# Kernel tuning notes

Measured on AMD Instinct MI355X. Metric: run time of the kernel, lower is better.

## Reference

```python
import jax, jax.numpy as jnp
import numpy as np

NUM_NODES = 100000
PROP_STEP = 8


def _spmm(vals, rows, cols, x):
    # sparse [N,N] @ dense [N,F]: gather source rows, scale, scatter-add to dest
    gathered = x[cols] * vals[:, None]  # [E, F]
    return jax.ops.segment_sum(gathered, rows, num_segments=NUM_NODES)


def setup_inputs() -> dict:
    key = jax.random.key(0)
    k1, k2, k3, k4, k5 = jax.random.split(key, 5)
    N, E, C = NUM_NODES, 3200000, 128
    x = jax.random.normal(k1, (N, C), dtype=jnp.float32)
    # xavier_uniform for weight [c_in, c_out]
    limit = float(np.sqrt(6.0 / (C + C)))
    weight = jax.random.uniform(k2, (C, C), dtype=jnp.float32, minval=-limit, maxval=limit)
    lap_vals = jax.random.uniform(k3, (E,), dtype=jnp.float32)
    lap_rows = jax.random.randint(k4, (E,), 0, N, dtype=jnp.int64)
    lap_cols = jax.random.randint(k5, (E,), 0, N, dtype=jnp.int64)
    return {"x": x, "weight": weight, "lap_vals": lap_vals,
            "lap_rows": lap_rows, "lap_cols": lap_cols}


def reference(x, weight, lap_vals, lap_rows, lap_cols):
    # filter_type='low', dropout inactive (eval / p=0)
    identity = x
    out = x @ weight  # [N, c_out]
    for _ in range(PROP_STEP):
        out = _spmm(lap_vals, lap_rows, lap_cols, out)
    return identity + out
```

## Files before the change

### kernel.cpp

```cpp
#include <hip/hip_runtime.h>
#include <hip/hip_bf16.h>
#include <hip/hip_fp16.h>
#include <stdint.h>

#define CCH 128
#define FINAL_SCALE 268435456.0f
#define RND 2048
#define BUKSH 9
#define BUKROWS 512
#define MAXBUK 256
#define COLMASK 0x1FFFF


__global__ __launch_bounds__(256) void bucket_hist_kernel(const int* __restrict__ rows,
                                                          int* __restrict__ bukcnt,
                                                          int E, int nbuk) {
    __shared__ int h[MAXBUK];
    for (int i = threadIdx.x; i < nbuk; i += 256) h[i] = 0;
    __syncthreads();
    int stride = gridDim.x * blockDim.x;
    for (int e = blockIdx.x * blockDim.x + threadIdx.x; e < E; e += stride)
        atomicAdd(&h[rows[e] >> BUKSH], 1);
    __syncthreads();
    for (int i = threadIdx.x; i < nbuk; i += 256)
        if (h[i]) atomicAdd(&bukcnt[i], h[i]);
}

__global__ __launch_bounds__(MAXBUK) void bucket_scan_kernel(const int* __restrict__ bukcnt,
                                                             int* __restrict__ bukptr,
                                                             int* __restrict__ gcur, int nbuk) {
    __shared__ int tile[MAXBUK];
    int t = threadIdx.x;
    tile[t] = (t < nbuk) ? bukcnt[t] : 0;
    __syncthreads();
    for (int off = 1; off < MAXBUK; off <<= 1) {
        int add = (t >= off) ? tile[t - off] : 0;
        __syncthreads();
        tile[t] += add;
        __syncthreads();
    }
    int excl = (t == 0) ? 0 : tile[t - 1];
    if (t < nbuk) {
        bukptr[t] = excl;
        gcur[t] = excl;
    }
    if (t == nbuk - 1) bukptr[nbuk] = tile[t];
}

__global__ __launch_bounds__(256) void part_kernel(const int* __restrict__ rows,
                                                   const int* __restrict__ cols,
                                                   const float* __restrict__ vals,
                                                   int* __restrict__ gcur,
                                                   unsigned int* __restrict__ rec_rc,
                                                   float* __restrict__ rec_v,
                                                   int E, int nbuk) {
    __shared__ int hist[MAXBUK];
    __shared__ int offs[MAXBUK];
    __shared__ int cur[MAXBUK];
    __shared__ int gbase[MAXBUK];
    __shared__ unsigned int stage_rc[RND];
    __shared__ float stage_v[RND];
    __shared__ unsigned char stage_b[RND];

    int base = blockIdx.x * RND;
    int cnt = E - base;
    if (cnt > RND) cnt = RND;
    if (cnt <= 0) return;

    for (int i = threadIdx.x; i < nbuk; i += 256) hist[i] = 0;
    __syncthreads();

    int myr[RND / 256], myc[RND / 256];
    float myv[RND / 256];
#pragma unroll
    for (int k = 0; k < RND / 256; ++k) {
        int li = k * 256 + threadIdx.x;
        bool ok = li < cnt;
        int gi = base + li;
        myr[k] = ok ? rows[gi] : -1;
        myc[k] = ok ? cols[gi] : 0;
        myv[k] = ok ? vals[gi] : 0.f;
        if (ok) atomicAdd(&hist[myr[k] >> BUKSH], 1);
    }
    __syncthreads();

    if (threadIdx.x == 0) {
        int run = 0;
        for (int b = 0; b < nbuk; ++b) {
            offs[b] = run;
            cur[b] = run;
            run += hist[b];
        }
    }
    __syncthreads();
    if (threadIdx.x < nbuk) gbase[threadIdx.x] = atomicAdd(&gcur[threadIdx.x], hist[threadIdx.x]);
    __syncthreads();

#pragma unroll
    for (int k = 0; k < RND / 256; ++k) {
        if (myr[k] >= 0) {
            int b = myr[k] >> BUKSH;
            int p = atomicAdd(&cur[b], 1);
            stage_rc[p] = ((unsigned int)(myr[k] & (BUKROWS - 1)) << 17) | (unsigned int)myc[k];
            stage_v[p] = myv[k];
            stage_b[p] = (unsigned char)b;
        }
    }
    __syncthreads();

    for (int i = threadIdx.x; i < cnt; i += 256) {
        int b = stage_b[i];
        size_t d = (size_t)gbase[b] + (i - offs[b]);
        rec_rc[d] = stage_rc[i];
        rec_v[d] = stage_v[i];
    }
}

__global__ __launch_bounds__(512) void csrfill2_kernel(const unsigned int* __restrict__ rec_rc,
                                                       const float* __restrict__ rec_v,
                                                       const int* __restrict__ bukptr,
                                                       int* __restrict__ row_ptr,
                                                       int2* __restrict__ edges,
                                                       int n, int E) {
    __shared__ int lcnt[BUKROWS];
    __shared__ int lscan[BUKROWS];
    __shared__ int lfill[BUKROWS];
    int bucket = blockIdx.x;
    int r0 = bucket << BUKSH;
    if (r0 >= n) return;
    int t = threadIdx.x;
    int bstart = bukptr[bucket];
    int bend = bukptr[bucket + 1];

    lcnt[t] = 0;
    __syncthreads();

    for (int i = bstart + t; i < bend; i += 512)
        atomicAdd(&lcnt[rec_rc[i] >> 17], 1);
    __syncthreads();

    int v = lcnt[t];
    lscan[t] = v;
    __syncthreads();
    for (int off = 1; off < 512; off <<= 1) {
        int add = (t >= off) ? lscan[t - off] : 0;
        __syncthreads();
        lscan[t] += add;
        __syncthreads();
    }
    int excl = lscan[t] - v;

    int r = r0 + t;
    if (r < n) row_ptr[r] = bstart + excl;
    if (bucket == 0 && t == 0) row_ptr[n] = E;

    lfill[t] = 0;
    lcnt[t] = bstart + excl;
    __syncthreads();

    int i = bstart + t;
    for (; i + 512 < bend; i += 1024) {
        unsigned int wa = rec_rc[i];
        unsigned int wb = rec_rc[i + 512];
        float va = rec_v[i];
        float vb = rec_v[i + 512];
        int ra = wa >> 17, rb = wb >> 17;
        int pa = lcnt[ra] + atomicAdd(&lfill[ra], 1);
        int pb = lcnt[rb] + atomicAdd(&lfill[rb], 1);
        edges[pa] = make_int2((int)(wa & COLMASK), __float_as_int(va));
        edges[pb] = make_int2((int)(wb & COLMASK), __float_as_int(vb));
    }
    if (i < bend) {
        unsigned int wa = rec_rc[i];
        float va = rec_v[i];
        int ra = wa >> 17;
        int pa = lcnt[ra] + atomicAdd(&lfill[ra], 1);
        edges[pa] = make_int2((int)(wa & COLMASK), __float_as_int(va));
    }
}


#define GEMM_ROWS 64

__global__ __launch_bounds__(256) void gemm_kernel(const float* __restrict__ x,
                                                   const float* __restrict__ w,
                                                   __half* __restrict__ out, int n) {
    __shared__ __half2 wl[CCH * 64];
    for (int i = threadIdx.x; i < CCH * 64 / 2; i += 256) {
        float4 v = ((const float4*)w)[i];
        wl[2 * i]     = __float22half2_rn(make_float2(v.x, v.y));
        wl[2 * i + 1] = __float22half2_rn(make_float2(v.z, v.w));
    }
    __syncthreads();

    int tc = threadIdx.x & 31;
    int tr = threadIdx.x >> 5;
    int rbase = blockIdx.x * GEMM_ROWS + tr * 8;
    int nr = n - rbase;
    if (nr > 8) nr = 8;
    if (nr <= 0) nr = 0;

    float acc[8][4] = {};
    const float* xp = x + (size_t)rbase * CCH;

    float4 xc[8];
#pragma unroll
    for (int j = 0; j < 8; ++j)
        xc[j] = (j < nr) ? *(const float4*)(xp + (size_t)j * CCH)
                         : make_float4(0.f, 0.f, 0.f, 0.f);

    for (int k = 0; k < CCH; k += 4) {
        float4 xn[8];
        if (k + 4 < CCH) {
#pragma unroll
            for (int j = 0; j < 8; ++j)
                xn[j] = (j < nr) ? *(const float4*)(xp + (size_t)j * CCH + k + 4)
                                 : make_float4(0.f, 0.f, 0.f, 0.f);
        }
#pragma unroll
        for (int kk = 0; kk < 4; ++kk) {
            __half2 w01 = wl[(k + kk) * 64 + tc * 2];
            __half2 w23 = wl[(k + kk) * 64 + tc * 2 + 1];
            float2 f01 = __half22float2(w01);
            float2 f23 = __half22float2(w23);
#pragma unroll
            for (int j = 0; j < 8; ++j) {
                float xs = (kk == 0) ? xc[j].x : (kk == 1) ? xc[j].y : (kk == 2) ? xc[j].z : xc[j].w;
                acc[j][0] += xs * f01.x;
                acc[j][1] += xs * f01.y;
                acc[j][2] += xs * f23.x;
                acc[j][3] += xs * f23.y;
            }
        }
        if (k + 4 < CCH) {
#pragma unroll
            for (int j = 0; j < 8; ++j) xc[j] = xn[j];
        }
    }
#pragma unroll
    for (int j = 0; j < 8; ++j)
        if (j < nr) {
            __half2* orow = (__half2*)(out + (size_t)(rbase + j) * CCH + tc * 4);
            orow[0] = __float22half2_rn(make_float2(acc[j][0], acc[j][1]));
            orow[1] = __float22half2_rn(make_float2(acc[j][2], acc[j][3]));
        }
}


template <int FINAL>
__global__ __launch_bounds__(256) void spmm_kernel(const int* __restrict__ row_ptr,
                                                   const int2* __restrict__ edges,
                                                   const __half* __restrict__ src,
                                                   __half* __restrict__ dsth,
                                                   float* __restrict__ dstf,
                                                   const float* __restrict__ identity,
                                                   int n) {
    int lane = threadIdx.x & 63;
    int row = (blockIdx.x * blockDim.x + threadIdx.x) >> 6;
    if (row >= n) return;
    int g = lane >> 4;
    int gl = lane & 15;

    int s = row_ptr[row];
    int e = row_ptr[row + 1];

    float acc[8] = {};

    for (int base = s; base < e; base += 16) {
        int2 ed[4];
        float4 gv[4];
#pragma unroll
        for (int t = 0; t < 4; ++t) {
            int idx = base + g * 4 + t;
            bool ok = idx < e;
            ed[t] = edges[ok ? idx : s];
            if (!ok) ed[t].y = 0;
        }
#pragma unroll
        for (int t = 0; t < 4; ++t)
            gv[t] = *(const float4*)(src + (size_t)ed[t].x * CCH + gl * 8);
#pragma unroll
        for (int t = 0; t < 4; ++t) {
            float v = __int_as_float(ed[t].y);
            const __half* h = (const __half*)&gv[t];
#pragma unroll
            for (int j = 0; j < 8; ++j)
                acc[j] += v * __half2float(h[j]);
        }
    }

#pragma unroll
    for (int j = 0; j < 8; ++j) {
        acc[j] += __shfl_xor(acc[j], 16, 64);
        acc[j] += __shfl_xor(acc[j], 32, 64);
    }

    if (FINAL) {
        if (g == 0) {
            const float* iv = identity + (size_t)row * CCH + gl * 8;
            float4 o;
            o.x = iv[0] + acc[0] * FINAL_SCALE;
            o.y = iv[1] + acc[1] * FINAL_SCALE;
            o.z = iv[2] + acc[2] * FINAL_SCALE;
            o.w = iv[3] + acc[3] * FINAL_SCALE;
            *(float4*)(dstf + (size_t)row * CCH + gl * 8) = o;
        } else if (g == 1) {
            const float* iv = identity + (size_t)row * CCH + gl * 8 + 4;
            float4 o;
            o.x = iv[0] + acc[4] * FINAL_SCALE;
            o.y = iv[1] + acc[5] * FINAL_SCALE;
            o.z = iv[2] + acc[6] * FINAL_SCALE;
            o.w = iv[3] + acc[7] * FINAL_SCALE;
            *(float4*)(dstf + (size_t)row * CCH + gl * 8 + 4) = o;
        }
    } else {
        if (g == 0) {
            __half2 h[4];
            h[0] = __float22half2_rn(make_float2(acc[0] * 0.0625f, acc[1] * 0.0625f));
            h[1] = __float22half2_rn(make_float2(acc[2] * 0.0625f, acc[3] * 0.0625f));
            h[2] = __float22half2_rn(make_float2(acc[4] * 0.0625f, acc[5] * 0.0625f));
            h[3] = __float22half2_rn(make_float2(acc[6] * 0.0625f, acc[7] * 0.0625f));
            *(float4*)(dsth + (size_t)row * CCH + gl * 8) = *(float4*)h;
        }
    }
}


static inline size_t align256(size_t x) { return (x + 255) & ~(size_t)255; }

extern "C" void kernel_launch(void* const* d_in, const int* in_sizes, int n_in,
                              void* d_out, int out_size, void* d_ws, size_t ws_size,
                              hipStream_t stream) {
    const float* x = (const float*)d_in[0];
    const float* w = (const float*)d_in[1];
    const float* lap_vals = (const float*)d_in[2];
    const int* lap_rows = (const int*)d_in[3];
    const int* lap_cols = (const int*)d_in[4];

    const int N = in_sizes[0] / CCH;
    const int E = in_sizes[2];
    const int NBUK = (N + BUKROWS - 1) >> BUKSH;

    char* ws = (char*)d_ws;
    size_t off = 0;
    __half* bufA = (__half*)(ws + off); off = align256(off + (size_t)N * CCH * sizeof(__half));
    __half* bufB = (__half*)(ws + off); off = align256(off + (size_t)N * CCH * sizeof(__half));
    int2* edges = (int2*)(ws + off);    off = align256(off + (size_t)E * sizeof(int2) + 16);
    int* row_ptr = (int*)(ws + off);    off = align256(off + (size_t)(N + 1) * sizeof(int));
    int* bukcnt = (int*)(ws + off);     off = align256(off + (size_t)MAXBUK * sizeof(int));
    int* bukptr = (int*)(ws + off);     off = align256(off + (size_t)(MAXBUK + 1) * sizeof(int));
    int* gcur = (int*)(ws + off);       off = align256(off + (size_t)MAXBUK * sizeof(int));
    (void)ws_size;
    unsigned int* rec_rc = (unsigned int*)bufA;
    float* rec_v = (float*)(rec_rc + E);

    float* out = (float*)d_out;

    hipMemsetAsync(bukcnt, 0, (size_t)MAXBUK * sizeof(int), stream);

    bucket_hist_kernel<<<512, 256, 0, stream>>>(lap_rows, bukcnt, E, NBUK);
    bucket_scan_kernel<<<1, MAXBUK, 0, stream>>>(bukcnt, bukptr, gcur, NBUK);
    part_kernel<<<(E + RND - 1) / RND, 256, 0, stream>>>(lap_rows, lap_cols, lap_vals,
                                                         gcur, rec_rc, rec_v, E, NBUK);
    csrfill2_kernel<<<NBUK, 512, 0, stream>>>(rec_rc, rec_v, bukptr, row_ptr, edges, N, E);

    gemm_kernel<<<(N + GEMM_ROWS - 1) / GEMM_ROWS, 256, 0, stream>>>(x, w, bufA, N);

    int spmm_blocks = (N + 3) / 4;
    const __half* src = bufA;
    __half* dst = bufB;
    for (int step = 1; step <= 7; ++step) {
        spmm_kernel<0><<<spmm_blocks, 256, 0, stream>>>(row_ptr, edges, src, dst, nullptr, nullptr, N);
        __half* t = (__half*)src;
        src = dst;
        dst = t;
    }
    spmm_kernel<1><<<spmm_blocks, 256, 0, stream>>>(row_ptr, edges, src, nullptr, out, x, N);
}
```

Measured before the change: 1.135 ms.

## Split SpMM feature dimension into two half-width passes per step

Each propagation step now launches the SpMM kernel twice, each pass gathering and writing only 64 of the 128 fp16 feature channels. This halves the size of the gathered working set per pass, aiming for better cache hit rates on the random row gathers. In exchange the CSR row pointers and edge list are read twice per step, launch count doubles, and each gather becomes an 8-byte load instead of 16 bytes.

```diff
diff --git a/kernel.cpp b/kernel.cpp
--- a/kernel.cpp
+++ b/kernel.cpp
@@ -254,7 +254,7 @@
                                                    __half* __restrict__ dsth,
                                                    float* __restrict__ dstf,
                                                    const float* __restrict__ identity,
-                                                   int n) {
+                                                   int n, int half) {
     int lane = threadIdx.x & 63;
     int row = (blockIdx.x * blockDim.x + threadIdx.x) >> 6;
     if (row >= n) return;
@@ -264,11 +264,12 @@
     int s = row_ptr[row];
     int e = row_ptr[row + 1];
 
-    float acc[8] = {};
+    float acc[4] = {};
+    const __half* srcg = src + half * 64 + gl * 4;
 
     for (int base = s; base < e; base += 16) {
         int2 ed[4];
-        float4 gv[4];
+        float2 gv[4];
 #pragma unroll
         for (int t = 0; t < 4; ++t) {
             int idx = base + g * 4 + t;
@@ -278,49 +279,41 @@
         }
 #pragma unroll
         for (int t = 0; t < 4; ++t)
-            gv[t] = *(const float4*)(src + (size_t)ed[t].x * CCH + gl * 8);
+            gv[t] = *(const float2*)(srcg + (size_t)ed[t].x * CCH);
 #pragma unroll
         for (int t = 0; t < 4; ++t) {
             float v = __int_as_float(ed[t].y);
             const __half* h = (const __half*)&gv[t];
 #pragma unroll
-            for (int j = 0; j < 8; ++j)
+            for (int j = 0; j < 4; ++j)
                 acc[j] += v * __half2float(h[j]);
         }
     }
 
 #pragma unroll
-    for (int j = 0; j < 8; ++j) {
+    for (int j = 0; j < 4; ++j) {
         acc[j] += __shfl_xor(acc[j], 16, 64);
         acc[j] += __shfl_xor(acc[j], 32, 64);
     }
 
     if (FINAL) {
         if (g == 0) {
-            const float* iv = identity + (size_t)row * CCH + gl * 8;
+            const float* iv = identity + (size_t)row * CCH + half * 64 + gl * 4;
             float4 o;
             o.x = iv[0] + acc[0] * FINAL_SCALE;
             o.y = iv[1] + acc[1] * FINAL_SCALE;
             o.z = iv[2] + acc[2] * FINAL_SCALE;
             o.w = iv[3] + acc[3] * FINAL_SCALE;
-            *(float4*)(dstf + (size_t)row * CCH + gl * 8) = o;
-        } else if (g == 1) {
-            const float* iv = identity + (size_t)row * CCH + gl * 8 + 4;
-            float4 o;
-            o.x = iv[0] + acc[4] * FINAL_SCALE;
-            o.y = iv[1] + acc[5] * FINAL_SCALE;
-            o.z = iv[2] + acc[6] * FINAL_SCALE;
-            o.w = iv[3] + acc[7] * FINAL_SCALE;
-            *(float4*)(dstf + (size_t)row * CCH + gl * 8 + 4) = o;
+            *(float4*)(dstf + (size_t)row * CCH + half * 64 + gl * 4) = o;
         }
     } else {
         if (g == 0) {
-            __half2 h[4];
-            h[0] = __float22half2_rn(make_float2(acc[0] * 0.0625f, acc[1] * 0.0625f));
-            h[1] = __float22half2_rn(make_float2(acc[2] * 0.0625f, acc[3] * 0.0625f));
-            h[2] = __float22half2_rn(make_float2(acc[4] * 0.0625f, acc[5] * 0.0625f));
-            h[3] = __float22half2_rn(make_float2(acc[6] * 0.0625f, acc[7] * 0.0625f));
-            *(float4*)(dsth + (size_t)row * CCH + gl * 8) = *(float4*)h;
+            __half2 h01 = __float22half2_rn(make_float2(acc[0] * 0.0625f, acc[1] * 0.0625f));
+            __half2 h23 = __float22half2_rn(make_float2(acc[2] * 0.0625f, acc[3] * 0.0625f));
+            float2 hv;
+            ((__half2*)&hv)[0] = h01;
+            ((__half2*)&hv)[1] = h23;
+            *(float2*)(dsth + (size_t)row * CCH + half * 64 + gl * 4) = hv;
         }
     }
 }
@@ -370,10 +363,12 @@
     const __half* src = bufA;
     __half* dst = bufB;
     for (int step = 1; step <= 7; ++step) {
-        spmm_kernel<0><<<spmm_blocks, 256, 0, stream>>>(row_ptr, edges, src, dst, nullptr, nullptr, N);
+        spmm_kernel<0><<<spmm_blocks, 256, 0, stream>>>(row_ptr, edges, src, dst, nullptr, nullptr, N, 0);
+        spmm_kernel<0><<<spmm_blocks, 256, 0, stream>>>(row_ptr, edges, src, dst, nullptr, nullptr, N, 1);
         __half* t = (__half*)src;
         src = dst;
         dst = t;
     }
-    spmm_kernel<1><<<spmm_blocks, 256, 0, stream>>>(row_ptr, edges, src, nullptr, out, x, N);
-}
+    spmm_kernel<1><<<spmm_blocks, 256, 0, stream>>>(row_ptr, edges, src, nullptr, out, x, N, 0);
+    spmm_kernel<1><<<spmm_blocks, 256, 0, stream>>>(row_ptr, edges, src, nullptr, out, x, N, 1);
+}
```

Result: slower. 1.290 ms (+13.7%).

## Use fp16 MFMA instructions for the dense x@W GEMM

Applied to the files above, without the earlier changes.

Replaces the scalar FMA register-tiled GEMM with a matrix-core version. Each wave computes a 16x128 output tile using mfma_f32_16x16x32_f16, with W stored transposed as fp16 in padded shared memory. The aim is to cut the GEMM's compute time, which is a small part of the pipeline next to the eight SpMM passes. Inputs are now rounded to fp16 before the multiply, and the output stores are scattered 2-byte writes.

```diff
diff --git a/kernel.cpp b/kernel.cpp
--- a/kernel.cpp
+++ b/kernel.cpp
@@ -180,70 +180,82 @@
 }
 
 
-#define GEMM_ROWS 64
+typedef _Float16 f16x8 __attribute__((ext_vector_type(8)));
+typedef float f32x4 __attribute__((ext_vector_type(4)));
+typedef short s4_t __attribute__((ext_vector_type(4)));
+
+#define WT_LD 136
 
 __global__ __launch_bounds__(256) void gemm_kernel(const float* __restrict__ x,
                                                    const float* __restrict__ w,
                                                    __half* __restrict__ out, int n) {
-    __shared__ __half2 wl[CCH * 64];
-    for (int i = threadIdx.x; i < CCH * 64 / 2; i += 256) {
-        float4 v = ((const float4*)w)[i];
-        wl[2 * i]     = __float22half2_rn(make_float2(v.x, v.y));
-        wl[2 * i + 1] = __float22half2_rn(make_float2(v.z, v.w));
-    }
-    __syncthreads();
-
-    int tc = threadIdx.x & 31;
-    int tr = threadIdx.x >> 5;
-    int rbase = blockIdx.x * GEMM_ROWS + tr * 8;
-    int nr = n - rbase;
-    if (nr > 8) nr = 8;
-    if (nr <= 0) nr = 0;
-
-    float acc[8][4] = {};
-    const float* xp = x + (size_t)rbase * CCH;
-
-    float4 xc[8];
-#pragma unroll
-    for (int j = 0; j < 8; ++j)
-        xc[j] = (j < nr) ? *(const float4*)(xp + (size_t)j * CCH)
-                         : make_float4(0.f, 0.f, 0.f, 0.f);
-
-    for (int k = 0; k < CCH; k += 4) {
-        float4 xn[8];
-        if (k + 4 < CCH) {
-#pragma unroll
-            for (int j = 0; j < 8; ++j)
-                xn[j] = (j < nr) ? *(const float4*)(xp + (size_t)j * CCH + k + 4)
-                                 : make_float4(0.f, 0.f, 0.f, 0.f);
-        }
-#pragma unroll
-        for (int kk = 0; kk < 4; ++kk) {
-            __half2 w01 = wl[(k + kk) * 64 + tc * 2];
-            __half2 w23 = wl[(k + kk) * 64 + tc * 2 + 1];
-            float2 f01 = __half22float2(w01);
-            float2 f23 = __half22float2(w23);
-#pragma unroll
-            for (int j = 0; j < 8; ++j) {
-                float xs = (kk == 0) ? xc[j].x : (kk == 1) ? xc[j].y : (kk == 2) ? xc[j].z : xc[j].w;
-                acc[j][0] += xs * f01.x;
-                acc[j][1] += xs * f01.y;
-                acc[j][2] += xs * f23.x;
-                acc[j][3] += xs * f23.y;
-            }
-        }
-        if (k + 4 < CCH) {
-#pragma unroll
-            for (int j = 0; j < 8; ++j) xc[j] = xn[j];
-        }
-    }
-#pragma unroll
-    for (int j = 0; j < 8; ++j)
-        if (j < nr) {
-            __half2* orow = (__half2*)(out + (size_t)(rbase + j) * CCH + tc * 4);
-            orow[0] = __float22half2_rn(make_float2(acc[j][0], acc[j][1]));
-            orow[1] = __float22half2_rn(make_float2(acc[j][2], acc[j][3]));
-        }
+    __shared__ _Float16 wt[CCH * WT_LD];
+    int tid = threadIdx.x;
+#pragma unroll
+    for (int i = 0; i < 16; ++i) {
+        int idx = i * 256 + tid;
+        float4 v = ((const float4*)w)[idx];
+        int k = idx >> 5;
+        int c0 = (idx & 31) << 2;
+        wt[(c0 + 0) * WT_LD + k] = (_Float16)v.x;
+        wt[(c0 + 1) * WT_LD + k] = (_Float16)v.y;
+        wt[(c0 + 2) * WT_LD + k] = (_Float16)v.z;
+        wt[(c0 + 3) * WT_LD + k] = (_Float16)v.w;
+    }
+    __syncthreads();
+
+    int lane = tid & 63;
+    int wave = tid >> 6;
+    int lr = lane & 15;
+    int lg = lane >> 4;
+    int rbase = blockIdx.x * 64 + wave * 16;
+
+    f16x8 a[4];
+    int arow = rbase + lr;
+    if (arow < n) {
+        const float* xp = x + (size_t)arow * CCH;
+#pragma unroll
+        for (int kt = 0; kt < 4; ++kt) {
+            float4 f0 = *(const float4*)(xp + kt * 32 + lg * 4);
+            float4 f1 = *(const float4*)(xp + kt * 32 + 16 + lg * 4);
+            f16x8 a8;
+            a8[0] = (_Float16)f0.x; a8[1] = (_Float16)f0.y;
+            a8[2] = (_Float16)f0.z; a8[3] = (_Float16)f0.w;
+            a8[4] = (_Float16)f1.x; a8[5] = (_Float16)f1.y;
+            a8[6] = (_Float16)f1.z; a8[7] = (_Float16)f1.w;
+            a[kt] = a8;
+        }
+    } else {
+        f16x8 z = {};
+#pragma unroll
+        for (int kt = 0; kt < 4; ++kt) a[kt] = z;
+    }
+
+    f32x4 acc[8];
+#pragma unroll
+    for (int ct = 0; ct < 8; ++ct) acc[ct] = (f32x4){0.f, 0.f, 0.f, 0.f};
+
+#pragma unroll
+    for (int ct = 0; ct < 8; ++ct) {
+        const _Float16* bp = &wt[(ct * 16 + lr) * WT_LD];
+#pragma unroll
+        for (int kt = 0; kt < 4; ++kt) {
+            union { s4_t s[2]; f16x8 h; } u;
+            u.s[0] = *(const s4_t*)(bp + kt * 32 + lg * 4);
+            u.s[1] = *(const s4_t*)(bp + kt * 32 + 16 + lg * 4);
+            acc[ct] = __builtin_amdgcn_mfma_f32_16x16x32_f16(a[kt], u.h, acc[ct], 0, 0, 0);
+        }
+    }
+
+#pragma unroll
+    for (int ct = 0; ct < 8; ++ct) {
+#pragma unroll
+        for (int reg = 0; reg < 4; ++reg) {
+            int orow = rbase + lg * 4 + reg;
+            if (orow < n)
+                out[(size_t)orow * CCH + ct * 16 + lr] = __float2half(acc[ct][reg]);
+        }
+    }
 }
 
 
@@ -364,7 +376,7 @@
                                                          gcur, rec_rc, rec_v, E, NBUK);
     csrfill2_kernel<<<NBUK, 512, 0, stream>>>(rec_rc, rec_v, bukptr, row_ptr, edges, N, E);
 
-    gemm_kernel<<<(N + GEMM_ROWS - 1) / GEMM_ROWS, 256, 0, stream>>>(x, w, bufA, N);
+    gemm_kernel<<<(N + 63) / 64, 256, 0, stream>>>(x, w, bufA, N);
 
     int spmm_blocks = (N + 3) / 4;
     const __half* src = bufA;
```

After: 1.083 ms. 1.05x faster.
